# Kernel optimization log

Hardware: AMD Instinct MI355X
Metric: run time of the kernel (lower is better)

Reference implementation:

```python
import jax, jax.numpy as jnp
import numpy as np

N_NODES = 100000
N_EDGES = 1000000
F_IN = 256
HID = 256
HID2 = 128
N_CLS = 2


def setup_inputs() -> dict:
    key = jax.random.key(0)
    ks = jax.random.split(key, 8)
    x = jax.random.normal(ks[0], (N_NODES, F_IN), dtype=jnp.float32)
    edge_index = jax.random.randint(ks[1], (2, N_EDGES), 0, N_NODES, dtype=jnp.int64)
    s = lambda k, shp: jax.random.normal(k, shp, dtype=jnp.float32) / np.sqrt(shp[0])
    return {
        "x": x,
        "edge_index": edge_index,
        "W1l": s(ks[2], (F_IN, HID)),
        "W1r": s(ks[3], (F_IN, HID)),
        "b1": jnp.zeros((HID,), jnp.float32),
        "W2l": s(ks[4], (HID, HID2)),
        "W2r": s(ks[5], (HID, HID2)),
        "b2": jnp.zeros((HID2,), jnp.float32),
        "Wc": s(ks[6], (HID2, N_CLS)),
        "bc": jnp.zeros((N_CLS,), jnp.float32),
    }


def _sage_conv(x, src, dst, deg_inv, Wl, Wr, b):
    # mean-aggregate neighbor (source) features at each destination node
    msg = x[src]                                              # [E, F]
    agg = jax.ops.segment_sum(msg, dst, num_segments=N_NODES)  # [N, F]
    mean = agg * deg_inv[:, None]                             # zero for isolated nodes
    return mean @ Wl + b + x @ Wr


def reference(x, edge_index, W1l, W1r, b1, W2l, W2r, b2, Wc, bc):
    src, dst = edge_index[0], edge_index[1]
    cnt = jax.ops.segment_sum(jnp.ones((N_EDGES,), x.dtype), dst, num_segments=N_NODES)
    deg_inv = jnp.where(cnt > 0, 1.0 / jnp.maximum(cnt, 1.0), 0.0)
    h = jax.nn.relu(_sage_conv(x, src, dst, deg_inv, W1l, W1r, b1))   # dropout is identity in eval
    h = jax.nn.relu(_sage_conv(h, src, dst, deg_inv, W2l, W2r, b2))
    logits = h @ Wc + bc
    return jax.nn.log_softmax(logits, axis=1)
```

## Files before the change

kernel.cpp:

```cpp
#include <hip/hip_runtime.h>
#include <hip/hip_bf16.h>

#define NN 100000
#define NE 1000000
#define MPAD 100096
#define MT64  1564
#define MTP64 1568

typedef __attribute__((ext_vector_type(8))) short bf16x8;
typedef __attribute__((ext_vector_type(4))) float f32x4;
typedef __attribute__((ext_vector_type(2))) float f32x2;
typedef __attribute__((ext_vector_type(8))) unsigned short us8;

static __device__ __forceinline__ float bf2f(unsigned short u){
  unsigned int x = ((unsigned int)u) << 16;
  return __uint_as_float(x);
}
static __device__ __forceinline__ unsigned short f2bf(float f){
  unsigned int x = __float_as_uint(f);
  unsigned int r = (x + 0x7fffu + ((x >> 16) & 1u)) >> 16;
  return (unsigned short)r;
}
static __device__ __forceinline__ void addv(float* acc, us8 v){
  #pragma unroll
  for (int k = 0; k < 8; k++) acc[k] += bf2f(v[k]);
}
static __device__ __forceinline__ unsigned char f2fp8(float f){
  unsigned int u = __float_as_uint(f);
  unsigned int s = (u >> 24) & 0x80u;
  float av = fabsf(f);
  if (av >= 448.f) return (unsigned char)(s | 0x7Eu);
  if (av < 0.015625f){
    int m = (int)(av * 512.0f + 0.5f);
    return (unsigned char)(s | (unsigned)m);
  }
  unsigned int au = u & 0x7FFFFFFFu;
  unsigned int r = au + 0x7FFFFu + ((au >> 20) & 1u);
  return (unsigned char)(s | ((r >> 20) - 960u));
}
#if !__has_builtin(__builtin_amdgcn_cvt_pk_f32_fp8)
static __device__ __forceinline__ float fp8tof(unsigned char b){
  unsigned int s = ((unsigned int)(b & 0x80u)) << 24;
  unsigned int e = (b >> 3) & 0xFu, m = b & 7u;
  float v = (e == 0) ? ((float)m * 0.001953125f)
                     : __uint_as_float(((e + 120u) << 23) | (m << 20));
  return __uint_as_float(__float_as_uint(v) | s);
}
#endif
static __device__ __forceinline__ void addq(float* acc, uint2 v){
#if __has_builtin(__builtin_amdgcn_cvt_pk_f32_fp8)
  f32x2 p0 = __builtin_amdgcn_cvt_pk_f32_fp8((int)v.x, false);
  f32x2 p1 = __builtin_amdgcn_cvt_pk_f32_fp8((int)v.x, true);
  f32x2 p2 = __builtin_amdgcn_cvt_pk_f32_fp8((int)v.y, false);
  f32x2 p3 = __builtin_amdgcn_cvt_pk_f32_fp8((int)v.y, true);
  acc[0] += p0[0]; acc[1] += p0[1]; acc[2] += p1[0]; acc[3] += p1[1];
  acc[4] += p2[0]; acc[5] += p2[1]; acc[6] += p3[0]; acc[7] += p3[1];
#else
  unsigned int a = v.x, b = v.y;
  acc[0] += fp8tof(a & 0xFF);         acc[1] += fp8tof((a >> 8) & 0xFF);
  acc[2] += fp8tof((a >> 16) & 0xFF); acc[3] += fp8tof(a >> 24);
  acc[4] += fp8tof(b & 0xFF);         acc[5] += fp8tof((b >> 8) & 0xFF);
  acc[6] += fp8tof((b >> 16) & 0xFF); acc[7] += fp8tof(b >> 24);
#endif
}
static __device__ __forceinline__ void gld16(const void* g, void* l){
  __builtin_amdgcn_global_load_lds((const __attribute__((address_space(1))) void*)g,
                                   (__attribute__((address_space(3))) void*)l, 16, 0, 0);
}


__global__ void k_degree(const int* __restrict__ dst, int* __restrict__ cnt, int E){
  int e = blockIdx.x * blockDim.x + threadIdx.x;
  if (e < E) atomicAdd(&cnt[dst[e]], 1);
}

__global__ void k_chunk_sum(const int* __restrict__ cnt, int* __restrict__ partials, int N){
  __shared__ int sw[16];
  int b = blockIdx.x, t = threadIdx.x;
  int i = b * 1024 + t;
  int v = (i < N) ? cnt[i] : 0;
  #pragma unroll
  for (int off = 32; off; off >>= 1) v += __shfl_xor(v, off);
  int lane = t & 63, w = t >> 6;
  if (lane == 0) sw[w] = v;
  __syncthreads();
  if (t < 16){
    int s = sw[t];
    #pragma unroll
    for (int off = 8; off; off >>= 1) s += __shfl_xor(s, off);
    if (t == 0) partials[b] = s;
  }
}

__global__ void k_chunk_scan(const int* __restrict__ cnt, const int* __restrict__ partials,
                             int nchunk,
                             int* __restrict__ offs, int* __restrict__ cursor,
                             float* __restrict__ deginv, int N){
  __shared__ int sd[1024];
  __shared__ int sp[128];
  int b = blockIdx.x, t = threadIdx.x;
  if (t < 128) sp[t] = (t < b && t < nchunk) ? partials[t] : 0;
  int i = b * 1024 + t;
  int v = (i < N) ? cnt[i] : 0;
  sd[t] = v;
  __syncthreads();
  #pragma unroll
  for (int off = 64; off; off >>= 1){
    if (t < off) sp[t] += sp[t + off];
    __syncthreads();
  }
  for (int off = 1; off < 1024; off <<= 1){
    int x = (t >= off) ? sd[t - off] : 0;
    __syncthreads();
    sd[t] += x;
    __syncthreads();
  }
  if (i < N){
    int excl = sp[0] + sd[t] - v;
    offs[i] = excl;
    cursor[i] = excl;
    deginv[i] = (v > 0) ? (1.0f / (float)v) : 0.0f;
  }
}

__global__ void k_fill(const int* __restrict__ src, const int* __restrict__ dst,
                       int* __restrict__ cursor, int* __restrict__ csr, int E){
  int e = blockIdx.x * blockDim.x + threadIdx.x;
  if (e < E){
    int p = atomicAdd(&cursor[dst[e]], 1);
    csr[p] = src[e];
  }
}


__global__ void k_cvt(const float* __restrict__ x, unsigned short* __restrict__ xb){
  size_t i = ((size_t)blockIdx.x * 256 + threadIdx.x) * 8;
  if (i >= (size_t)MPAD * 256) return;
  int row = (int)(i >> 8);
  us8 o;
  if (row < NN){
    const float4* p = (const float4*)(x + i);
    float4 a = p[0], b = p[1];
    o[0]=f2bf(a.x); o[1]=f2bf(a.y); o[2]=f2bf(a.z); o[3]=f2bf(a.w);
    o[4]=f2bf(b.x); o[5]=f2bf(b.y); o[6]=f2bf(b.z); o[7]=f2bf(b.w);
  } else {
    #pragma unroll
    for (int j = 0; j < 8; j++) o[j] = 0;
  }
  *(us8*)(xb + i) = o;
}


__global__ void k_prep_w(const float* __restrict__ W1l, const float* __restrict__ W1r,
                         const float* __restrict__ W2l, const float* __restrict__ W2r,
                         unsigned short* __restrict__ Bt1, unsigned short* __restrict__ Bt2){
  int i = blockIdx.x * 256 + threadIdx.x;
  if (i < 512 * 256){
    int n = i >> 8, k = i & 255;
    float v = (n < 256) ? W1l[k * 256 + n] : W1r[k * 256 + (n - 256)];
    Bt1[n * 256 + k] = f2bf(v);
  }
  if (i < 256 * 256){
    int n = i >> 8, k = i & 255;
    float v = (n < 128) ? W2l[k * 128 + n] : W2r[k * 128 + (n - 128)];
    Bt2[n * 256 + k] = f2bf(v);
  }
}


template<int NTL2, bool SPLIT>
__global__ __launch_bounds__(64)
void k_gemm(const unsigned short* __restrict__ A,
            const unsigned short* __restrict__ Bt,
            unsigned short* __restrict__ C,
            unsigned char* __restrict__ Q8)
{
  const int bid = blockIdx.x;
  const int xcd = bid & 7, j = bid >> 3;
  const int mt  = xcd * (MTP64 / 8) + (j >> NTL2);
  if (mt >= MT64) return;
  const int nt  = j & ((1 << NTL2) - 1);
  const int m0  = mt * 64;
  const int n0  = nt * 64;
  const int Nout = 64 << NTL2;

  __shared__ __align__(16) unsigned short lA[64 * 64];
  __shared__ __align__(16) unsigned short lB[64 * 64];
  const int lane = threadIdx.x & 63;

  f32x4 acc[4][4] = {};

  const int srow = lane >> 3;
  const int sc   = (lane & 7) ^ ((lane >> 3) & 7);

  for (int kt = 0; kt < 4; ++kt){
    asm volatile("s_waitcnt lgkmcnt(0)" ::: "memory");
    #pragma unroll
    for (int s = 0; s < 8; ++s){
      int row = s * 8 + srow;
      gld16(A  + (size_t)(m0 + row) * 256 + kt * 64 + sc * 8, &lA[s * 512]);
      gld16(Bt + (size_t)(n0 + row) * 256 + kt * 64 + sc * 8, &lB[s * 512]);
    }
    asm volatile("s_waitcnt vmcnt(0)" ::: "memory");
    __builtin_amdgcn_sched_barrier(0);
    #pragma unroll
    for (int ks = 0; ks < 2; ++ks){
      bf16x8 av[4], bv[4];
      const int kc = ks * 4 + (lane >> 4);
      #pragma unroll
      for (int m = 0; m < 4; m++){
        int r = m * 16 + (lane & 15);
        av[m] = *(const bf16x8*)&lA[r * 64 + ((kc ^ (r & 7)) << 3)];
      }
      #pragma unroll
      for (int n = 0; n < 4; n++){
        int c = n * 16 + (lane & 15);
        bv[n] = *(const bf16x8*)&lB[c * 64 + ((kc ^ (c & 7)) << 3)];
      }
      #pragma unroll
      for (int m = 0; m < 4; m++)
        #pragma unroll
        for (int n = 0; n < 4; n++)
          acc[m][n] = __builtin_amdgcn_mfma_f32_16x16x32_bf16(av[m], bv[n], acc[m][n], 0, 0, 0);
    }
  }

  const int crow0 = m0 + (lane >> 4) * 4;
  const int ccol0 = n0 + (lane & 15);
  if (SPLIT && n0 < 256){
    #pragma unroll
    for (int m = 0; m < 4; m++){
      #pragma unroll
      for (int r = 0; r < 4; r++){
        size_t rowoff = (size_t)(crow0 + m * 16 + r) * 256;
        #pragma unroll
        for (int n = 0; n < 4; n++)
          Q8[rowoff + ccol0 + n * 16] = f2fp8(acc[m][n][r]);
      }
    }
  } else {
    const int stride = SPLIT ? 256 : Nout;
    const int cbase  = SPLIT ? (ccol0 - 256) : ccol0;
    #pragma unroll
    for (int m = 0; m < 4; m++){
      #pragma unroll
      for (int r = 0; r < 4; r++){
        size_t rowoff = (size_t)(crow0 + m * 16 + r) * stride;
        #pragma unroll
        for (int n = 0; n < 4; n++)
          C[rowoff + cbase + n * 16] = f2bf(acc[m][n][r]);
      }
    }
  }
}


__global__ void k_agg1(const unsigned char* __restrict__ Q8,
                       const unsigned short* __restrict__ R1,
                       const float* __restrict__ b1,
                       const int* __restrict__ offs, const int* __restrict__ cnt,
                       const float* __restrict__ deginv,
                       const int* __restrict__ csr,
                       unsigned short* __restrict__ h, int N)
{
  int wv = threadIdx.x >> 6, lane = threadIdx.x & 63;
  int n = blockIdx.x * 4 + wv;
  if (n >= N) return;
  int beg = offs[n], d = cnt[n];
  const int g = lane >> 5;
  const int cl = lane & 31;
  const unsigned char* Qb = Q8 + cl * 8;

  float acc[8];
  #pragma unroll
  for (int k = 0; k < 8; k++) acc[k] = 0.f;

  for (int w0 = 0; w0 < d; w0 += 64){
    int wlen = min(d - w0, 64);
    int idx = 0;
    if (lane < wlen) idx = csr[beg + w0 + lane];
    int nIter = (wlen + 15) >> 4;
    for (int t = 0; t < nIter; t++){
      int e0 = t * 16 + g;
      int s0 = __shfl(idx, e0);
      int s1 = __shfl(idx, e0 + 2);
      int s2 = __shfl(idx, e0 + 4);
      int s3 = __shfl(idx, e0 + 6);
      int s4 = __shfl(idx, e0 + 8);
      int s5 = __shfl(idx, e0 + 10);
      int s6 = __shfl(idx, e0 + 12);
      int s7 = __shfl(idx, e0 + 14);
      uint2 v0 = *(const uint2*)(Qb + (size_t)s0 * 256);
      uint2 v1 = *(const uint2*)(Qb + (size_t)s1 * 256);
      uint2 v2 = *(const uint2*)(Qb + (size_t)s2 * 256);
      uint2 v3 = *(const uint2*)(Qb + (size_t)s3 * 256);
      uint2 v4 = *(const uint2*)(Qb + (size_t)s4 * 256);
      uint2 v5 = *(const uint2*)(Qb + (size_t)s5 * 256);
      uint2 v6 = *(const uint2*)(Qb + (size_t)s6 * 256);
      uint2 v7 = *(const uint2*)(Qb + (size_t)s7 * 256);
      if (e0 < wlen)      addq(acc, v0);
      if (e0 + 2 < wlen)  addq(acc, v1);
      if (e0 + 4 < wlen)  addq(acc, v2);
      if (e0 + 6 < wlen)  addq(acc, v3);
      if (e0 + 8 < wlen)  addq(acc, v4);
      if (e0 + 10 < wlen) addq(acc, v5);
      if (e0 + 12 < wlen) addq(acc, v6);
      if (e0 + 14 < wlen) addq(acc, v7);
    }
  }
  #pragma unroll
  for (int k = 0; k < 8; k++) acc[k] += __shfl_xor(acc[k], 32);

  if (lane < 32){
    float di = deginv[n];
    us8 rv = *(const us8*)(R1 + (size_t)n * 256 + cl * 8);
    float4 b0 = *(const float4*)(b1 + cl * 8);
    float4 b4 = *(const float4*)(b1 + cl * 8 + 4);
    float bb[8] = {b0.x, b0.y, b0.z, b0.w, b4.x, b4.y, b4.z, b4.w};
    us8 o;
    #pragma unroll
    for (int k = 0; k < 8; k++)
      o[k] = f2bf(fmaxf(acc[k] * di + bf2f(rv[k]) + bb[k], 0.f));
    *(us8*)(h + (size_t)n * 256 + cl * 8) = o;
  }
}


__global__ void k_agg2cls(const unsigned short* __restrict__ C2,
                          const float* __restrict__ b2,
                          const float* __restrict__ Wc,
                          const float* __restrict__ bc,
                          const int* __restrict__ offs, const int* __restrict__ cnt,
                          const float* __restrict__ deginv,
                          const int* __restrict__ csr,
                          float* __restrict__ out, int N)
{
  int wv = threadIdx.x >> 6, lane = threadIdx.x & 63;
  int n = blockIdx.x * 4 + wv;
  if (n >= N) return;
  int beg = offs[n], d = cnt[n];
  const int g = lane >> 4;
  const int cl = lane & 15;

  float acc[8];
  #pragma unroll
  for (int k = 0; k < 8; k++) acc[k] = 0.f;

  for (int w0 = 0; w0 < d; w0 += 64){
    int wlen = min(d - w0, 64);
    int idx = 0;
    if (lane < wlen) idx = csr[beg + w0 + lane];
    int nIter = (wlen + 31) >> 5;
    for (int t = 0; t < nIter; t++){
      int e0 = t * 32 + g;
      int s0 = __shfl(idx, e0);
      int s1 = __shfl(idx, e0 + 4);
      int s2 = __shfl(idx, e0 + 8);
      int s3 = __shfl(idx, e0 + 12);
      int s4 = __shfl(idx, e0 + 16);
      int s5 = __shfl(idx, e0 + 20);
      int s6 = __shfl(idx, e0 + 24);
      int s7 = __shfl(idx, e0 + 28);
      us8 v0 = *(const us8*)(C2 + (size_t)s0 * 256 + cl * 8);
      us8 v1 = *(const us8*)(C2 + (size_t)s1 * 256 + cl * 8);
      us8 v2 = *(const us8*)(C2 + (size_t)s2 * 256 + cl * 8);
      us8 v3 = *(const us8*)(C2 + (size_t)s3 * 256 + cl * 8);
      us8 v4 = *(const us8*)(C2 + (size_t)s4 * 256 + cl * 8);
      us8 v5 = *(const us8*)(C2 + (size_t)s5 * 256 + cl * 8);
      us8 v6 = *(const us8*)(C2 + (size_t)s6 * 256 + cl * 8);
      us8 v7 = *(const us8*)(C2 + (size_t)s7 * 256 + cl * 8);
      if (e0 < wlen)      addv(acc, v0);
      if (e0 + 4 < wlen)  addv(acc, v1);
      if (e0 + 8 < wlen)  addv(acc, v2);
      if (e0 + 12 < wlen) addv(acc, v3);
      if (e0 + 16 < wlen) addv(acc, v4);
      if (e0 + 20 < wlen) addv(acc, v5);
      if (e0 + 24 < wlen) addv(acc, v6);
      if (e0 + 28 < wlen) addv(acc, v7);
    }
  }
  #pragma unroll
  for (int k = 0; k < 8; k++){
    acc[k] += __shfl_xor(acc[k], 16);
    acc[k] += __shfl_xor(acc[k], 32);
  }

  float di = deginv[n];
  us8 rv = *(const us8*)(C2 + (size_t)n * 256 + 128 + cl * 8);
  float4 b0 = *(const float4*)(b2 + cl * 8);
  float4 b4 = *(const float4*)(b2 + cl * 8 + 4);
  float bb[8] = {b0.x, b0.y, b0.z, b0.w, b4.x, b4.y, b4.z, b4.w};
  float p0 = 0.f, p1 = 0.f;
  #pragma unroll
  for (int k = 0; k < 8; k += 2){
    float h0 = fmaxf(acc[k]     * di + bf2f(rv[k])     + bb[k],     0.f);
    float h1 = fmaxf(acc[k + 1] * di + bf2f(rv[k + 1]) + bb[k + 1], 0.f);
    float4 w = *(const float4*)(Wc + (cl * 8 + k) * 2);
    p0 += h0 * w.x + h1 * w.z;
    p1 += h0 * w.y + h1 * w.w;
  }
  #pragma unroll
  for (int off = 8; off; off >>= 1){
    p0 += __shfl_xor(p0, off);
    p1 += __shfl_xor(p1, off);
  }
  if (lane == 0){
    float z0 = p0 + bc[0], z1 = p1 + bc[1];
    float m = fmaxf(z0, z1);
    float lse = m + logf(expf(z0 - m) + expf(z1 - m));
    out[(size_t)n * 2 + 0] = z0 - lse;
    out[(size_t)n * 2 + 1] = z1 - lse;
  }
}


extern "C" void kernel_launch(void* const* d_in, const int* in_sizes, int n_in,
                              void* d_out, int out_size, void* d_ws, size_t ws_size,
                              hipStream_t stream)
{
  const float* x   = (const float*)d_in[0];
  const int*   ei  = (const int*)d_in[1];
  const float* W1l = (const float*)d_in[2];
  const float* W1r = (const float*)d_in[3];
  const float* b1  = (const float*)d_in[4];
  const float* W2l = (const float*)d_in[5];
  const float* W2r = (const float*)d_in[6];
  const float* b2  = (const float*)d_in[7];
  const float* Wc  = (const float*)d_in[8];
  const float* bc  = (const float*)d_in[9];
  float* out = (float*)d_out;

  const int N = NN, E = NE;
  const int* src = ei;
  const int* dst = ei + E;

  char* ws = (char*)d_ws;
  size_t off = 0;
  auto alloc = [&](size_t bytes) -> void* {
    void* p = ws + off;
    off += (bytes + 255) & ~(size_t)255;
    return p;
  };
  int*   cnt      = (int*)alloc((size_t)N * 4);
  int*   offs     = (int*)alloc((size_t)N * 4);
  int*   cursor   = (int*)alloc((size_t)N * 4);
  float* deginv   = (float*)alloc((size_t)N * 4);
  int*   partials = (int*)alloc(1024);
  int*   csr      = (int*)alloc((size_t)E * 4);
  unsigned short* Bt1 = (unsigned short*)alloc((size_t)512 * 256 * 2);
  unsigned short* Bt2 = (unsigned short*)alloc((size_t)256 * 256 * 2);
  unsigned short* xb  = (unsigned short*)alloc((size_t)MPAD * 256 * 2);
  unsigned char*  Q8  = (unsigned char*)alloc((size_t)MPAD * 256);
  unsigned short* R1  = (unsigned short*)alloc((size_t)MPAD * 256 * 2);

  unsigned short* h  = xb;
  unsigned short* C2 = R1;

  (void)in_sizes; (void)n_in; (void)out_size; (void)ws_size;

  hipMemsetAsync(cnt, 0, (size_t)N * 4, stream);

  int nchunk = (N + 1023) / 1024;
  k_degree<<<(E + 255) / 256, 256, 0, stream>>>(dst, cnt, E);
  k_chunk_sum<<<nchunk, 1024, 0, stream>>>(cnt, partials, N);
  k_chunk_scan<<<nchunk, 1024, 0, stream>>>(cnt, partials, nchunk, offs, cursor, deginv, N);
  k_fill<<<(E + 255) / 256, 256, 0, stream>>>(src, dst, cursor, csr, E);

  k_cvt<<<MPAD / 8, 256, 0, stream>>>(x, xb);
  k_prep_w<<<512, 256, 0, stream>>>(W1l, W1r, W2l, W2r, Bt1, Bt2);

  k_gemm<3, true><<<MTP64 * 8, 64, 0, stream>>>(xb, Bt1, R1, Q8);
  k_agg1<<<N / 4, 256, 0, stream>>>(Q8, R1, b1, offs, cnt, deginv, csr, h, N);

  k_gemm<2, false><<<MTP64 * 4, 64, 0, stream>>>(h, Bt2, C2, (unsigned char*)nullptr);
  k_agg2cls<<<N / 4, 256, 0, stream>>>(C2, b2, Wc, bc, offs, cnt, deginv, csr, out, N);
}
```

Measured before the change: 349.0 us.

## Co-schedule independent preprocessing kernels into shared launches to overlap work

Merges degree counting, x-to-bf16 conversion and weight transposition into one launch whose block indices are interleaved by role. Also merges the CSR fill kernel with the first GEMM, interleaving atomic-scatter blocks with MFMA GEMM blocks. The aim is to overlap latency-bound atomic work with bandwidth- or compute-bound work and to cut kernel launch overhead. The cost is more complex block-role dispatch, and the GEMM kernel now carries a larger parameter set. The LDS footprint is allocated even for the fill blocks, which may limit occupancy for that part.

```diff
diff --git a/kernel.cpp b/kernel.cpp
--- a/kernel.cpp
+++ b/kernel.cpp
@@ -6,6 +6,10 @@
 #define MPAD 100096
 #define MT64  1564
 #define MTP64 1568
+#define NG1   (MTP64 * 8)
+#define NFB   (NE / 64)
+#define NDB   ((NE + 255) / 256)
+#define NCB   (MPAD / 8)
 
 typedef __attribute__((ext_vector_type(8))) short bf16x8;
 typedef __attribute__((ext_vector_type(4))) float f32x4;
@@ -69,10 +73,57 @@
 }
 
 
-__global__ void k_degree(const int* __restrict__ dst, int* __restrict__ cnt, int E){
-  int e = blockIdx.x * blockDim.x + threadIdx.x;
-  if (e < E) atomicAdd(&cnt[dst[e]], 1);
-}
+__global__ __launch_bounds__(256)
+void k_dc(const int* __restrict__ dst, int* __restrict__ cnt,
+          const float* __restrict__ x, unsigned short* __restrict__ xb,
+          const float* __restrict__ W1l, const float* __restrict__ W1r,
+          const float* __restrict__ W2l, const float* __restrict__ W2r,
+          unsigned short* __restrict__ Bt1, unsigned short* __restrict__ Bt2)
+{
+  const int bid = blockIdx.x, t = threadIdx.x;
+  int role, idx;
+  if (bid < 2 * NDB){
+    role = bid & 1;
+    idx = bid >> 1;
+  } else if (bid < NDB + NCB){
+    role = 0; idx = bid - NDB;
+  } else {
+    role = 2; idx = bid - NDB - NCB;
+  }
+
+  if (role == 1){
+    int e = idx * 256 + t;
+    if (e < NE) atomicAdd(&cnt[dst[e]], 1);
+  } else if (role == 0){
+    size_t i = ((size_t)idx * 256 + t) * 8;
+    if (i >= (size_t)MPAD * 256) return;
+    int row = (int)(i >> 8);
+    us8 o;
+    if (row < NN){
+      const float4* p = (const float4*)(x + i);
+      float4 a = p[0], b = p[1];
+      o[0]=f2bf(a.x); o[1]=f2bf(a.y); o[2]=f2bf(a.z); o[3]=f2bf(a.w);
+      o[4]=f2bf(b.x); o[5]=f2bf(b.y); o[6]=f2bf(b.z); o[7]=f2bf(b.w);
+    } else {
+      #pragma unroll
+      for (int j = 0; j < 8; j++) o[j] = 0;
+    }
+    *(us8*)(xb + i) = o;
+  } else {
+    int i = idx * 256 + t;
+    if (i < 512 * 256){
+      int n = i >> 8, k = i & 255;
+      float v = (n < 256) ? W1l[k * 256 + n] : W1r[k * 256 + (n - 256)];
+      Bt1[n * 256 + k] = f2bf(v);
+    }
+    if (i < 256 * 256){
+      int n = i >> 8, k = i & 255;
+      float v = (n < 128) ? W2l[k * 128 + n] : W2r[k * 128 + (n - 128)];
+      Bt2[n * 256 + k] = f2bf(v);
+    }
+  }
+}
+
 
 __global__ void k_chunk_sum(const int* __restrict__ cnt, int* __restrict__ partials, int N){
   __shared__ int sw[16];
@@ -123,57 +174,114 @@
   }
 }
 
-__global__ void k_fill(const int* __restrict__ src, const int* __restrict__ dst,
-                       int* __restrict__ cursor, int* __restrict__ csr, int E){
-  int e = blockIdx.x * blockDim.x + threadIdx.x;
-  if (e < E){
-    int p = atomicAdd(&cursor[dst[e]], 1);
-    csr[p] = src[e];
-  }
-}
-
-
-__global__ void k_cvt(const float* __restrict__ x, unsigned short* __restrict__ xb){
-  size_t i = ((size_t)blockIdx.x * 256 + threadIdx.x) * 8;
-  if (i >= (size_t)MPAD * 256) return;
-  int row = (int)(i >> 8);
-  us8 o;
-  if (row < NN){
-    const float4* p = (const float4*)(x + i);
-    float4 a = p[0], b = p[1];
-    o[0]=f2bf(a.x); o[1]=f2bf(a.y); o[2]=f2bf(a.z); o[3]=f2bf(a.w);
-    o[4]=f2bf(b.x); o[5]=f2bf(b.y); o[6]=f2bf(b.z); o[7]=f2bf(b.w);
+
+__global__ __launch_bounds__(64)
+void k_fg(const unsigned short* __restrict__ A,
+          const unsigned short* __restrict__ Bt,
+          unsigned short* __restrict__ R1,
+          unsigned char* __restrict__ Q8,
+          const int* __restrict__ src, const int* __restrict__ dst,
+          int* __restrict__ cursor, int* __restrict__ csr)
+{
+  __shared__ __align__(16) unsigned short lA[64 * 64];
+  __shared__ __align__(16) unsigned short lB[64 * 64];
+  const int bid = blockIdx.x;
+  const int lane = threadIdx.x & 63;
+
+  bool isg; int idx;
+  if (bid < 2 * NG1){
+    isg = (bid & 15) < 8;
+    idx = ((bid >> 4) << 3) + (bid & 7);
   } else {
-    #pragma unroll
-    for (int j = 0; j < 8; j++) o[j] = 0;
-  }
-  *(us8*)(xb + i) = o;
-}
-
-
-__global__ void k_prep_w(const float* __restrict__ W1l, const float* __restrict__ W1r,
-                         const float* __restrict__ W2l, const float* __restrict__ W2r,
-                         unsigned short* __restrict__ Bt1, unsigned short* __restrict__ Bt2){
-  int i = blockIdx.x * 256 + threadIdx.x;
-  if (i < 512 * 256){
-    int n = i >> 8, k = i & 255;
-    float v = (n < 256) ? W1l[k * 256 + n] : W1r[k * 256 + (n - 256)];
-    Bt1[n * 256 + k] = f2bf(v);
-  }
-  if (i < 256 * 256){
-    int n = i >> 8, k = i & 255;
-    float v = (n < 128) ? W2l[k * 128 + n] : W2r[k * 128 + (n - 128)];
-    Bt2[n * 256 + k] = f2bf(v);
-  }
-}
-
-
-template<int NTL2, bool SPLIT>
+    isg = false; idx = bid - NG1;
+  }
+
+  if (!isg){
+    int e = idx * 64 + lane;
+    if (e < NE){
+      int p = atomicAdd(&cursor[dst[e]], 1);
+      csr[p] = src[e];
+    }
+    return;
+  }
+
+  const int xcd = idx & 7, j = idx >> 3;
+  const int mt  = xcd * (MTP64 / 8) + (j >> 3);
+  if (mt >= MT64) return;
+  const int nt  = j & 7;
+  const int m0  = mt * 64;
+  const int n0  = nt * 64;
+
+  f32x4 acc[4][4] = {};
+  const int srow = lane >> 3;
+  const int sc   = (lane & 7) ^ ((lane >> 3) & 7);
+
+  for (int kt = 0; kt < 4; ++kt){
+    asm volatile("s_waitcnt lgkmcnt(0)" ::: "memory");
+    #pragma unroll
+    for (int s = 0; s < 8; ++s){
+      int row = s * 8 + srow;
+      gld16(A  + (size_t)(m0 + row) * 256 + kt * 64 + sc * 8, &lA[s * 512]);
+      gld16(Bt + (size_t)(n0 + row) * 256 + kt * 64 + sc * 8, &lB[s * 512]);
+    }
+    asm volatile("s_waitcnt vmcnt(0)" ::: "memory");
+    __builtin_amdgcn_sched_barrier(0);
+    #pragma unroll
+    for (int ks = 0; ks < 2; ++ks){
+      bf16x8 av[4], bv[4];
+      const int kc = ks * 4 + (lane >> 4);
+      #pragma unroll
+      for (int m = 0; m < 4; m++){
+        int r = m * 16 + (lane & 15);
+        av[m] = *(const bf16x8*)&lA[r * 64 + ((kc ^ (r & 7)) << 3)];
+      }
+      #pragma unroll
+      for (int n = 0; n < 4; n++){
+        int c = n * 16 + (lane & 15);
+        bv[n] = *(const bf16x8*)&lB[c * 64 + ((kc ^ (c & 7)) << 3)];
+      }
+      #pragma unroll
+      for (int m = 0; m < 4; m++)
+        #pragma unroll
+        for (int n = 0; n < 4; n++)
+          acc[m][n] = __builtin_amdgcn_mfma_f32_16x16x32_bf16(av[m], bv[n], acc[m][n], 0, 0, 0);
+    }
+  }
+
+  const int crow0 = m0 + (lane >> 4) * 4;
+  const int ccol0 = n0 + (lane & 15);
+  if (n0 < 256){
+    #pragma unroll
+    for (int m = 0; m < 4; m++){
+      #pragma unroll
+      for (int r = 0; r < 4; r++){
+        size_t rowoff = (size_t)(crow0 + m * 16 + r) * 256;
+        #pragma unroll
+        for (int n = 0; n < 4; n++)
+          Q8[rowoff + ccol0 + n * 16] = f2fp8(acc[m][n][r]);
+      }
+    }
+  } else {
+    const int cbase = ccol0 - 256;
+    #pragma unroll
+    for (int m = 0; m < 4; m++){
+      #pragma unroll
+      for (int r = 0; r < 4; r++){
+        size_t rowoff = (size_t)(crow0 + m * 16 + r) * 256;
+        #pragma unroll
+        for (int n = 0; n < 4; n++)
+          R1[rowoff + cbase + n * 16] = f2bf(acc[m][n][r]);
+      }
+    }
+  }
+}
+
+
+template<int NTL2>
 __global__ __launch_bounds__(64)
 void k_gemm(const unsigned short* __restrict__ A,
             const unsigned short* __restrict__ Bt,
-            unsigned short* __restrict__ C,
-            unsigned char* __restrict__ Q8)
+            unsigned short* __restrict__ C)
 {
   const int bid = blockIdx.x;
   const int xcd = bid & 7, j = bid >> 3;
@@ -189,7 +297,6 @@
   const int lane = threadIdx.x & 63;
 
   f32x4 acc[4][4] = {};
-
   const int srow = lane >> 3;
   const int sc   = (lane & 7) ^ ((lane >> 3) & 7);
 
@@ -227,29 +334,14 @@
 
   const int crow0 = m0 + (lane >> 4) * 4;
   const int ccol0 = n0 + (lane & 15);
-  if (SPLIT && n0 < 256){
-    #pragma unroll
-    for (int m = 0; m < 4; m++){
-      #pragma unroll
-      for (int r = 0; r < 4; r++){
-        size_t rowoff = (size_t)(crow0 + m * 16 + r) * 256;
-        #pragma unroll
-        for (int n = 0; n < 4; n++)
-          Q8[rowoff + ccol0 + n * 16] = f2fp8(acc[m][n][r]);
-      }
-    }
-  } else {
-    const int stride = SPLIT ? 256 : Nout;
-    const int cbase  = SPLIT ? (ccol0 - 256) : ccol0;
-    #pragma unroll
-    for (int m = 0; m < 4; m++){
-      #pragma unroll
-      for (int r = 0; r < 4; r++){
-        size_t rowoff = (size_t)(crow0 + m * 16 + r) * stride;
-        #pragma unroll
-        for (int n = 0; n < 4; n++)
-          C[rowoff + cbase + n * 16] = f2bf(acc[m][n][r]);
-      }
+  #pragma unroll
+  for (int m = 0; m < 4; m++){
+    #pragma unroll
+    for (int r = 0; r < 4; r++){
+      size_t rowoff = (size_t)(crow0 + m * 16 + r) * Nout;
+      #pragma unroll
+      for (int n = 0; n < 4; n++)
+        C[rowoff + ccol0 + n * 16] = f2bf(acc[m][n][r]);
     }
   }
 }
@@ -460,18 +552,16 @@
 
   hipMemsetAsync(cnt, 0, (size_t)N * 4, stream);
 
+  k_dc<<<NDB + NCB + 512, 256, 0, stream>>>(dst, cnt, x, xb, W1l, W1r, W2l, W2r, Bt1, Bt2);
+
   int nchunk = (N + 1023) / 1024;
-  k_degree<<<(E + 255) / 256, 256, 0, stream>>>(dst, cnt, E);
   k_chunk_sum<<<nchunk, 1024, 0, stream>>>(cnt, partials, N);
   k_chunk_scan<<<nchunk, 1024, 0, stream>>>(cnt, partials, nchunk, offs, cursor, deginv, N);
-  k_fill<<<(E + 255) / 256, 256, 0, stream>>>(src, dst, cursor, csr, E);
-
-  k_cvt<<<MPAD / 8, 256, 0, stream>>>(x, xb);
-  k_prep_w<<<512, 256, 0, stream>>>(W1l, W1r, W2l, W2r, Bt1, Bt2);
-
-  k_gemm<3, true><<<MTP64 * 8, 64, 0, stream>>>(xb, Bt1, R1, Q8);
+
+  k_fg<<<NG1 + NFB, 64, 0, stream>>>(xb, Bt1, R1, Q8, src, dst, cursor, csr);
+
   k_agg1<<<N / 4, 256, 0, stream>>>(Q8, R1, b1, offs, cnt, deginv, csr, h, N);
 
-  k_gemm<2, false><<<MTP64 * 4, 64, 0, stream>>>(h, Bt2, C2, (unsigned char*)nullptr);
+  k_gemm<2><<<MTP64 * 4, 64, 0, stream>>>(h, Bt2, C2);
   k_agg2cls<<<N / 4, 256, 0, stream>>>(C2, b2, Wc, bc, offs, cnt, deginv, csr, out, N);
 }
```

Result: faster. 303.0 us (-13.2%).

## Fuse degree count, input convert, weight prep; partition CSR fill by destination range

Applied to the files above, without the earlier changes.

Merges the degree-count, x-to-bf16 conversion and weight transpose kernels into one launch that interleaves atomic-count blocks with convert blocks, so the atomic-bound and bandwidth-bound work can overlap and two launches disappear. The CSR fill is replaced by a version where each edge chunk is handled by 8 blocks, each inserting only edges whose destination falls in its eighth of the node range. This aims to localise atomics and CSR writes, at the cost of reading dst eight times.

```diff
diff --git a/kernel.cpp b/kernel.cpp
--- a/kernel.cpp
+++ b/kernel.cpp
@@ -6,6 +6,12 @@
 #define MPAD 100096
 #define MT64  1564
 #define MTP64 1568
+#define NG1   (MTP64 * 8)
+#define NDB   ((NE + 255) / 256)
+#define NCB   (MPAD / 8)
+#define NRES  (NN / 8)
+#define FCH   1024
+#define NFCH  ((NE + FCH - 1) / FCH)
 
 typedef __attribute__((ext_vector_type(8))) short bf16x8;
 typedef __attribute__((ext_vector_type(4))) float f32x4;
@@ -69,10 +75,57 @@
 }
 
 
-__global__ void k_degree(const int* __restrict__ dst, int* __restrict__ cnt, int E){
-  int e = blockIdx.x * blockDim.x + threadIdx.x;
-  if (e < E) atomicAdd(&cnt[dst[e]], 1);
-}
+__global__ __launch_bounds__(256)
+void k_dc(const int* __restrict__ dst, int* __restrict__ cnt,
+          const float* __restrict__ x, unsigned short* __restrict__ xb,
+          const float* __restrict__ W1l, const float* __restrict__ W1r,
+          const float* __restrict__ W2l, const float* __restrict__ W2r,
+          unsigned short* __restrict__ Bt1, unsigned short* __restrict__ Bt2)
+{
+  const int bid = blockIdx.x, t = threadIdx.x;
+  int role, idx;
+  if (bid < 2 * NDB){
+    role = bid & 1;
+    idx = bid >> 1;
+  } else if (bid < NDB + NCB){
+    role = 0; idx = bid - NDB;
+  } else {
+    role = 2; idx = bid - NDB - NCB;
+  }
+
+  if (role == 1){
+    int e = idx * 256 + t;
+    if (e < NE) atomicAdd(&cnt[dst[e]], 1);
+  } else if (role == 0){
+    size_t i = ((size_t)idx * 256 + t) * 8;
+    if (i >= (size_t)MPAD * 256) return;
+    int row = (int)(i >> 8);
+    us8 o;
+    if (row < NN){
+      const float4* p = (const float4*)(x + i);
+      float4 a = p[0], b = p[1];
+      o[0]=f2bf(a.x); o[1]=f2bf(a.y); o[2]=f2bf(a.z); o[3]=f2bf(a.w);
+      o[4]=f2bf(b.x); o[5]=f2bf(b.y); o[6]=f2bf(b.z); o[7]=f2bf(b.w);
+    } else {
+      #pragma unroll
+      for (int j = 0; j < 8; j++) o[j] = 0;
+    }
+    *(us8*)(xb + i) = o;
+  } else {
+    int i = idx * 256 + t;
+    if (i < 512 * 256){
+      int n = i >> 8, k = i & 255;
+      float v = (n < 256) ? W1l[k * 256 + n] : W1r[k * 256 + (n - 256)];
+      Bt1[n * 256 + k] = f2bf(v);
+    }
+    if (i < 256 * 256){
+      int n = i >> 8, k = i & 255;
+      float v = (n < 128) ? W2l[k * 128 + n] : W2r[k * 128 + (n - 128)];
+      Bt2[n * 256 + k] = f2bf(v);
+    }
+  }
+}
+
 
 __global__ void k_chunk_sum(const int* __restrict__ cnt, int* __restrict__ partials, int N){
   __shared__ int sw[16];
@@ -123,47 +176,26 @@
   }
 }
 
-__global__ void k_fill(const int* __restrict__ src, const int* __restrict__ dst,
-                       int* __restrict__ cursor, int* __restrict__ csr, int E){
-  int e = blockIdx.x * blockDim.x + threadIdx.x;
-  if (e < E){
-    int p = atomicAdd(&cursor[dst[e]], 1);
-    csr[p] = src[e];
-  }
-}
-
-
-__global__ void k_cvt(const float* __restrict__ x, unsigned short* __restrict__ xb){
-  size_t i = ((size_t)blockIdx.x * 256 + threadIdx.x) * 8;
-  if (i >= (size_t)MPAD * 256) return;
-  int row = (int)(i >> 8);
-  us8 o;
-  if (row < NN){
-    const float4* p = (const float4*)(x + i);
-    float4 a = p[0], b = p[1];
-    o[0]=f2bf(a.x); o[1]=f2bf(a.y); o[2]=f2bf(a.z); o[3]=f2bf(a.w);
-    o[4]=f2bf(b.x); o[5]=f2bf(b.y); o[6]=f2bf(b.z); o[7]=f2bf(b.w);
-  } else {
-    #pragma unroll
-    for (int j = 0; j < 8; j++) o[j] = 0;
-  }
-  *(us8*)(xb + i) = o;
-}
-
-
-__global__ void k_prep_w(const float* __restrict__ W1l, const float* __restrict__ W1r,
-                         const float* __restrict__ W2l, const float* __restrict__ W2r,
-                         unsigned short* __restrict__ Bt1, unsigned short* __restrict__ Bt2){
-  int i = blockIdx.x * 256 + threadIdx.x;
-  if (i < 512 * 256){
-    int n = i >> 8, k = i & 255;
-    float v = (n < 256) ? W1l[k * 256 + n] : W1r[k * 256 + (n - 256)];
-    Bt1[n * 256 + k] = f2bf(v);
-  }
-  if (i < 256 * 256){
-    int n = i >> 8, k = i & 255;
-    float v = (n < 128) ? W2l[k * 128 + n] : W2r[k * 128 + (n - 128)];
-    Bt2[n * 256 + k] = f2bf(v);
+
+__global__ __launch_bounds__(256)
+void k_fill_p(const int* __restrict__ src, const int* __restrict__ dst,
+              int* __restrict__ cursor, int* __restrict__ csr)
+{
+  const int bid = blockIdx.x;
+  const int r = bid & 7;
+  const int c = bid >> 3;
+  const int lo = r * NRES;
+  const int base = c * FCH;
+  #pragma unroll
+  for (int w = 0; w < FCH; w += 256){
+    int e = base + w + threadIdx.x;
+    if (e < NE){
+      int dn = dst[e];
+      if ((unsigned)(dn - lo) < (unsigned)NRES){
+        int p = atomicAdd(&cursor[dn], 1);
+        csr[p] = src[e];
+      }
+    }
   }
 }
 
@@ -189,7 +221,6 @@
   const int lane = threadIdx.x & 63;
 
   f32x4 acc[4][4] = {};
-
   const int srow = lane >> 3;
   const int sc   = (lane & 7) ^ ((lane >> 3) & 7);
 
@@ -209,13 +240,13 @@
       const int kc = ks * 4 + (lane >> 4);
       #pragma unroll
       for (int m = 0; m < 4; m++){
-        int r = m * 16 + (lane & 15);
-        av[m] = *(const bf16x8*)&lA[r * 64 + ((kc ^ (r & 7)) << 3)];
+        int rr = m * 16 + (lane & 15);
+        av[m] = *(const bf16x8*)&lA[rr * 64 + ((kc ^ (rr & 7)) << 3)];
       }
       #pragma unroll
       for (int n = 0; n < 4; n++){
-        int c = n * 16 + (lane & 15);
-        bv[n] = *(const bf16x8*)&lB[c * 64 + ((kc ^ (c & 7)) << 3)];
+        int cc = n * 16 + (lane & 15);
+        bv[n] = *(const bf16x8*)&lB[cc * 64 + ((kc ^ (cc & 7)) << 3)];
       }
       #pragma unroll
       for (int m = 0; m < 4; m++)
@@ -460,16 +491,16 @@
 
   hipMemsetAsync(cnt, 0, (size_t)N * 4, stream);
 
+  k_dc<<<NDB + NCB + 512, 256, 0, stream>>>(dst, cnt, x, xb, W1l, W1r, W2l, W2r, Bt1, Bt2);
+
   int nchunk = (N + 1023) / 1024;
-  k_degree<<<(E + 255) / 256, 256, 0, stream>>>(dst, cnt, E);
   k_chunk_sum<<<nchunk, 1024, 0, stream>>>(cnt, partials, N);
   k_chunk_scan<<<nchunk, 1024, 0, stream>>>(cnt, partials, nchunk, offs, cursor, deginv, N);
-  k_fill<<<(E + 255) / 256, 256, 0, stream>>>(src, dst, cursor, csr, E);
-
-  k_cvt<<<MPAD / 8, 256, 0, stream>>>(x, xb);
-  k_prep_w<<<512, 256, 0, stream>>>(W1l, W1r, W2l, W2r, Bt1, Bt2);
-
-  k_gemm<3, true><<<MTP64 * 8, 64, 0, stream>>>(xb, Bt1, R1, Q8);
+
+  k_fill_p<<<NFCH * 8, 256, 0, stream>>>(src, dst, cursor, csr);
+
+  k_gemm<3, true><<<NG1, 64, 0, stream>>>(xb, Bt1, R1, Q8);
+
   k_agg1<<<N / 4, 256, 0, stream>>>(Q8, R1, b1, offs, cnt, deginv, csr, h, N);
 
   k_gemm<2, false><<<MTP64 * 4, 64, 0, stream>>>(h, Bt2, C2, (unsigned char*)nullptr);
```

Measured after the change: 307.3 us. 11.9% less time.
